# Performance work log

Measured on AMD Instinct MI355X. Metric: run time of the kernel, lower is better.

Reference implementation:

```python
import jax, jax.numpy as jnp
import numpy as np
import math

L, N, Q, C, H = 6, 32, 100, 256, 8


def setup_inputs() -> dict:
    key = jax.random.key(0)
    k0, k1, k2 = jax.random.split(key, 3)
    hs_pair = jax.random.normal(k0, (L, N, Q, C), jnp.float32)
    xb = math.sqrt(6.0 / (C + 3 * C))  # xavier_uniform bound for (3C, C)
    in_proj_w = jax.random.uniform(k1, (3 * C, C), jnp.float32, -xb, xb)
    in_proj_b = jnp.zeros((3 * C,), jnp.float32)
    ob = 1.0 / math.sqrt(C)  # nn.Linear default bound
    out_w = jax.random.uniform(k2, (C, C), jnp.float32, -ob, ob)
    out_b = jnp.zeros((C,), jnp.float32)
    return {"hs_pair": hs_pair, "in_proj_w": in_proj_w, "in_proj_b": in_proj_b,
            "out_w": out_w, "out_b": out_b}


def _smha(q, k, v, ipw, ipb, ow, ob, mask=None):
    """Sigmoid multi-head attention (SMHA), batch-first.
    q: (N,T,E), k/v: (N,S,E), mask: (T,S) bool (True = masked -> attn 0).
    Returns (out (N,T,E), head-averaged pre-normalization sigmoid weights (N,T,S))."""
    E = q.shape[-1]
    Dh = E // H
    Nb, T, _ = q.shape
    S = k.shape[1]
    wq, wk, wv = ipw[:E], ipw[E:2 * E], ipw[2 * E:]
    bq, bk, bv = ipb[:E], ipb[E:2 * E], ipb[2 * E:]
    qh = (q @ wq.T + bq).reshape(Nb, T, H, Dh)
    kh = (k @ wk.T + bk).reshape(Nb, S, H, Dh)
    vh = (v @ wv.T + bv).reshape(Nb, S, H, Dh)
    scores = jnp.einsum('nthd,nshd->nhts', qh, kh) / jnp.sqrt(jnp.asarray(Dh, qh.dtype))
    attn = jax.nn.sigmoid(scores)
    if mask is not None:
        attn = jnp.where(mask[None, None], 0.0, attn)  # sigmoid(-inf) == 0
    out = jnp.einsum('nhts,nshd->nthd', attn / (attn.sum(-1, keepdims=True) + 1e-4), vh)
    out = out.reshape(Nb, T, E) @ ow.T + ob
    return out, attn.mean(axis=1)


def _sqdist(a, b):
    # a (...,M,C), b (...,K,C) -> squared euclidean (...,M,K); avoids (M,K,C) diff tensor
    return jnp.maximum(jnp.sum(a * a, -1)[..., :, None] + jnp.sum(b * b, -1)[..., None, :]
                       - 2.0 * jnp.einsum('...mc,...kc->...mk', a, b), 0.0)


def _forward(hs_pair, ipw, ipb, ow, ob):
    hs = hs_pair[-1]  # (N,Q,C)
    Nb = hs.shape[0]

    # mean_farthest_assignment over all layers: centers (L,N,2,C)
    c1_all = hs_pair.mean(2, keepdims=True)                      # (L,N,1,C)
    d_all = _sqdist(c1_all, hs_pair)[..., 0, :]                  # (L,N,Q); sq dist preserves argmax
    far_all = jnp.argmax(d_all, -1)
    c2_all = jnp.take_along_axis(hs_pair, far_all[..., None, None], axis=2)
    centers = jnp.concatenate([c1_all, c2_all], 2)               # (L,N,2,C)

    # global field: 2 centers attend to Q pair features
    mf, assignment = _smha(centers[-1], hs, hs, ipw, ipb, ow, ob)  # (N,2,C), (N,2,Q)
    card = assignment.sum(-1)                                      # (N,2)
    s_idx = jnp.argmin(card, -1)
    d_idx = jnp.argmax(card, -1)
    cd = jnp.take_along_axis(mf, d_idx[:, None, None], 1)[:, 0]    # (N,C)
    cs = jnp.take_along_axis(mf, s_idx[:, None, None], 1)[:, 0]

    # base_idx row j = (j..j+Q-2) mod Q, i.e. it excludes (j-1) mod Q
    excl = (jnp.arange(Q) - 1) % Q
    sum_all = hs.sum(1)                                            # (N,C)
    rows = jnp.arange(Q)

    def branch(kv, c1):
        # kv (N,S,C); c1 (N,Q,C) leave-one-out means; returns shift (N,Q)
        S = kv.shape[1]
        d = _sqdist(c1, kv)                                        # (N,Q,S)
        em = jnp.arange(S)[None, :] == excl[:, None]               # exclude col (j-1)%Q
        far = jnp.argmax(jnp.where(em[None], -jnp.inf, d), -1)     # (N,Q)
        c2 = jnp.take_along_axis(kv, far[..., None], axis=1)       # (N,Q,C)
        cen = jnp.stack([c1, c2], 2).reshape(Nb, 2 * Q, C)         # interleaved [c1_j, c2_j]
        m = jnp.zeros((2 * Q, S), bool).at[2 * rows, rows].set(True).at[2 * rows + 1, rows].set(True)
        mfx, asg = _smha(cen, kv, kv, ipw, ipb, ow, ob, mask=m)    # (N,2Q,C), (N,2Q,S)
        mfx = mfx.reshape(Nb, Q, 2, C)
        asg = asg.reshape(Nb, Q, 2, S)
        cardx = asg.sum(-1)                                        # (N,Q,2)
        si = jnp.argmin(cardx, -1)
        di = jnp.argmax(cardx, -1)
        cdx = jnp.take_along_axis(mfx, di[..., None, None], 2)[:, :, 0]  # (N,Q,C)
        csx = jnp.take_along_axis(mfx, si[..., None, None], 2)[:, :, 0]
        return (jnp.sqrt(jnp.sum((cdx - cd[:, None]) ** 2, -1) + 1e-12)
                + jnp.sqrt(jnp.sum((csx - cs[:, None]) ** 2, -1) + 1e-12))

    # remove-one branch
    c1_rm = (sum_all[:, None] - hs[:, excl]) / (Q - 1)
    shift_rm = branch(hs, c1_rm)

    # mean-displace branch: subset + batch-mean pseudo point appended
    mean_pair = hs.mean(1, keepdims=True)                          # (N,1,C)
    kv_md = jnp.concatenate([hs, mean_pair], 1)                    # (N,Q+1,C)
    c1_md = (sum_all[:, None] - hs[:, excl] + mean_pair) / Q
    shift_md = branch(kv_md, c1_md)

    return assignment, s_idx, d_idx, shift_rm, shift_md


def reference(hs_pair, in_proj_w, in_proj_b, out_w, out_b):
    return _forward(hs_pair, in_proj_w, in_proj_b, out_w, out_b)
```

## Files before the change

kernel.cpp:

```cpp
#include <hip/hip_runtime.h>
#include <math.h>

#define NB 32
#define QQ 100
#define CC 256
#define HH 8
#define DH 32
#define SM 101
#define TT 200
#define TB 400
#define PW 768

typedef __attribute__((ext_vector_type(8))) short s16x8;
typedef __attribute__((ext_vector_type(4))) float f32x4;

__device__ inline unsigned short f2bft(float x) {
    return (unsigned short)(__float_as_uint(x) >> 16);
}
__device__ inline ushort2 tsplit(float x) {
    unsigned u = __float_as_uint(x);
    float l = x - __uint_as_float(u & 0xffff0000u);
    ushort2 r;
    r.x = (unsigned short)(u >> 16);
    r.y = (unsigned short)(__float_as_uint(l) >> 16);
    return r;
}

__global__ __launch_bounds__(256)
void meanrow_kernel(const float* __restrict__ hs, float* __restrict__ meanF) {
    int n = blockIdx.x, cb = blockIdx.y;
    int tid = threadIdx.x;
    int c = cb * 128 + (tid & 127), rh = tid >> 7;
    __shared__ float part[2][128];
    const float* h = hs + (size_t)n * QQ * CC;
    float s = 0.f;
    for (int q = rh * 50; q < rh * 50 + 50; ++q) s += h[(size_t)q * CC + c];
    part[rh][tid & 127] = s;
    __syncthreads();
    if (rh == 0) meanF[(size_t)n * CC + c] = (part[0][tid & 127] + part[1][tid & 127]) * 0.01f;
}

#define LDK 40
__global__ __launch_bounds__(256, 2)
void gemm_mfma(const float* __restrict__ hs, const float* __restrict__ meanF,
               const float* __restrict__ W_g, const float* __restrict__ bias,
               float* __restrict__ out, int M, int Nout) {
    __shared__ unsigned short Ahs[128][LDK], Als[128][LDK], Bhs[128][LDK], Bls[128][LDK];
    int tid = threadIdx.x;
    int lane = tid & 63, wave = tid >> 6;
    int wm = (wave >> 1) * 64, wn = (wave & 1) * 64;
    int fr = lane & 15, kb = lane >> 4;
    int bm = blockIdx.x * 128, bn = blockIdx.y * 128;
    int srow = tid >> 1, scol = (tid & 1) * 16;
    int am = bm + srow; if (am >= M) am = M - 1;
    int an = am / SM, ar = am - an * SM;
    const float* pA = (ar < QQ) ? hs + ((size_t)an * QQ + ar) * CC + scol
                                : meanF + (size_t)an * CC + scol;
    const float* pW = W_g + (size_t)(bn + srow) * CC + scol;
    f32x4 acc[4][4];
#pragma unroll
    for (int mi = 0; mi < 4; ++mi)
#pragma unroll
        for (int ni = 0; ni < 4; ++ni)
            acc[mi][ni] = (f32x4){0.f, 0.f, 0.f, 0.f};
    for (int k0 = 0; k0 < CC; k0 += 32) {
        float4 av[4], wv[4];
#pragma unroll
        for (int j = 0; j < 4; ++j) {
            av[j] = *(const float4*)(pA + k0 + 4 * j);
            wv[j] = *(const float4*)(pW + k0 + 4 * j);
        }
        __syncthreads();
#pragma unroll
        for (int j = 0; j < 4; ++j) {
            ushort2 sx = tsplit(av[j].x), sy = tsplit(av[j].y), sz = tsplit(av[j].z), sw = tsplit(av[j].w);
            ushort4 h4; h4.x = sx.x; h4.y = sy.x; h4.z = sz.x; h4.w = sw.x;
            ushort4 l4; l4.x = sx.y; l4.y = sy.y; l4.z = sz.y; l4.w = sw.y;
            *(ushort4*)&Ahs[srow][scol + 4 * j] = h4;
            *(ushort4*)&Als[srow][scol + 4 * j] = l4;
            ushort2 tx = tsplit(wv[j].x), ty = tsplit(wv[j].y), tz = tsplit(wv[j].z), tw = tsplit(wv[j].w);
            ushort4 wh4; wh4.x = tx.x; wh4.y = ty.x; wh4.z = tz.x; wh4.w = tw.x;
            ushort4 wl4; wl4.x = tx.y; wl4.y = ty.y; wl4.z = tz.y; wl4.w = tw.y;
            *(ushort4*)&Bhs[srow][scol + 4 * j] = wh4;
            *(ushort4*)&Bls[srow][scol + 4 * j] = wl4;
        }
        __syncthreads();
        s16x8 fah[4], fal[4], fbh[4], fbl[4];
#pragma unroll
        for (int mi = 0; mi < 4; ++mi) {
            fah[mi] = *(const s16x8*)&Ahs[wm + mi * 16 + fr][kb * 8];
            fal[mi] = *(const s16x8*)&Als[wm + mi * 16 + fr][kb * 8];
        }
#pragma unroll
        for (int ni = 0; ni < 4; ++ni) {
            fbh[ni] = *(const s16x8*)&Bhs[wn + ni * 16 + fr][kb * 8];
            fbl[ni] = *(const s16x8*)&Bls[wn + ni * 16 + fr][kb * 8];
        }
#pragma unroll
        for (int mi = 0; mi < 4; ++mi)
#pragma unroll
            for (int ni = 0; ni < 4; ++ni) {
                acc[mi][ni] = __builtin_amdgcn_mfma_f32_16x16x32_bf16(fah[mi], fbh[ni], acc[mi][ni], 0, 0, 0);
                acc[mi][ni] = __builtin_amdgcn_mfma_f32_16x16x32_bf16(fah[mi], fbl[ni], acc[mi][ni], 0, 0, 0);
                acc[mi][ni] = __builtin_amdgcn_mfma_f32_16x16x32_bf16(fal[mi], fbh[ni], acc[mi][ni], 0, 0, 0);
            }
    }
#pragma unroll
    for (int mi = 0; mi < 4; ++mi) {
        int mb = bm + wm + mi * 16 + kb * 4;
#pragma unroll
        for (int r = 0; r < 4; ++r) {
            int m = mb + r;
            if (m < M) {
#pragma unroll
                for (int ni = 0; ni < 4; ++ni) {
                    int col = bn + wn + ni * 16 + fr;
                    out[(size_t)m * Nout + col] = acc[mi][ni][r] + bias[col];
                }
            }
        }
    }
}

__global__ __launch_bounds__(512, 2)
void gramfar(const float* __restrict__ hs, const float* __restrict__ meanF,
             const float* __restrict__ P_all, float* __restrict__ Psum0,
             int* __restrict__ far0, int* __restrict__ far_rm,
             int* __restrict__ far_md) {
    int n = blockIdx.x;
    int tid = threadIdx.x;
    int wave = tid >> 6, lane = tid & 63;
    int fr = lane & 15, kb = lane >> 4;
    __shared__ float G[SM][104];
    __shared__ unsigned short Ah[112][LDK], Al[112][LDK];
    __shared__ float sumdot[104], meandot[104], norm[104];
    __shared__ float psumP[2][CC];
    {
        int c = tid & 255, half = tid >> 8;
        const float* basep = P_all + (size_t)n * SM * PW + c;
        float accp = 0.f;
        for (int q = half * 50; q < half * 50 + 50; ++q) accp += basep[(size_t)q * PW];
        psumP[half][c] = accp;
    }
    __syncthreads();
    if (tid < 256) Psum0[(size_t)n * CC + tid] = psumP[0][tid] + psumP[1][tid];
    const float* hb = hs + (size_t)n * QQ * CC;
    const float* mb = meanF + (size_t)n * CC;
    f32x4 acc[7];
#pragma unroll
    for (int u = 0; u < 7; ++u) acc[u] = (f32x4){0.f, 0.f, 0.f, 0.f};
    for (int k0 = 0; k0 < CC; k0 += 32) {
        __syncthreads();
        if (tid < 224) {
            int row = tid >> 1, kk = (tid & 1) * 16;
            float4 v[4];
            if (row < SM) {
                const float* rp = (row < QQ) ? hb + (size_t)row * CC : mb;
#pragma unroll
                for (int j = 0; j < 4; ++j) v[j] = *(const float4*)(rp + k0 + kk + 4 * j);
            } else {
#pragma unroll
                for (int j = 0; j < 4; ++j) v[j] = (float4){0.f, 0.f, 0.f, 0.f};
            }
#pragma unroll
            for (int j = 0; j < 4; ++j) {
                ushort2 sx = tsplit(v[j].x), sy = tsplit(v[j].y), sz = tsplit(v[j].z), sw = tsplit(v[j].w);
                ushort4 h4; h4.x = sx.x; h4.y = sy.x; h4.z = sz.x; h4.w = sw.x;
                ushort4 l4; l4.x = sx.y; l4.y = sy.y; l4.z = sz.y; l4.w = sw.y;
                *(ushort4*)&Ah[row][kk + 4 * j] = h4;
                *(ushort4*)&Al[row][kk + 4 * j] = l4;
            }
        }
        __syncthreads();
#pragma unroll
        for (int u = 0; u < 7; ++u) {
            int tl = wave + u * 8;
            if (tl < 49) {
                int ti = tl / 7, tj = tl % 7;
                s16x8 ah = *(const s16x8*)&Ah[ti * 16 + fr][kb * 8];
                s16x8 al = *(const s16x8*)&Al[ti * 16 + fr][kb * 8];
                s16x8 bh = *(const s16x8*)&Ah[tj * 16 + fr][kb * 8];
                s16x8 bl = *(const s16x8*)&Al[tj * 16 + fr][kb * 8];
                acc[u] = __builtin_amdgcn_mfma_f32_16x16x32_bf16(ah, bh, acc[u], 0, 0, 0);
                acc[u] = __builtin_amdgcn_mfma_f32_16x16x32_bf16(ah, bl, acc[u], 0, 0, 0);
                acc[u] = __builtin_amdgcn_mfma_f32_16x16x32_bf16(al, bh, acc[u], 0, 0, 0);
            }
        }
    }
    __syncthreads();
#pragma unroll
    for (int u = 0; u < 7; ++u) {
        int tl = wave + u * 8;
        if (tl < 49) {
            int ti = tl / 7, tj = tl % 7;
#pragma unroll
            for (int r = 0; r < 4; ++r) {
                int m = ti * 16 + kb * 4 + r;
                int col = tj * 16 + fr;
                if (m < SM && col < SM) G[m][col] = acc[u][r];
            }
        }
    }
    __syncthreads();
    for (int s = tid; s < SM; s += 512) {
        float a = 0.f;
        for (int q = 0; q < QQ; ++q) a += G[s][q];
        sumdot[s] = a; meandot[s] = G[s][QQ]; norm[s] = G[s][s];
    }
    __syncthreads();
    if (tid < QQ) {
        int q = tid, qm1 = (q + QQ - 1) % QQ;
        const float* gq = G[qm1];
        int best = -1; float bv = -1e30f;
        for (int s = 0; s < QQ; ++s) {
            if (s == qm1) continue;
            float val = norm[s] - (sumdot[s] - gq[s]) * (2.f / 99.f);
            if (val > bv) { bv = val; best = s; }
        }
        far_rm[n * QQ + q] = best;
    } else if (tid >= 128 && tid < 128 + QQ) {
        int q = tid - 128, qm1 = (q + QQ - 1) % QQ;
        const float* gq = G[qm1];
        int best = -1; float bv = -1e30f;
        for (int s = 0; s < SM; ++s) {
            if (s == qm1) continue;
            float val = norm[s] - (sumdot[s] - gq[s] + meandot[s]) * (2.f / 100.f);
            if (val > bv) { bv = val; best = s; }
        }
        far_md[n * QQ + q] = best;
    } else if (tid == 256) {
        int best = 0; float bv = -1e30f;
        for (int q = 0; q < QQ; ++q) {
            float val = norm[q] - 0.02f * sumdot[q];
            if (val > bv) { bv = val; best = q; }
        }
        far0[n] = best;
    }
}

__global__ __launch_bounds__(512)
void smhaB_kernel(const float* __restrict__ P_all, const int* __restrict__ far0,
                  const float* __restrict__ ow, const float* __restrict__ ob,
                  float* __restrict__ out_assign, float* __restrict__ out_sidx,
                  float* __restrict__ out_didx, float* __restrict__ cd,
                  float* __restrict__ cs) {
    int n = blockIdx.x;
    int tid = threadIdx.x;
    int h = tid >> 6, lane = tid & 63;
    __shared__ float at[HH][2][104];
    __shared__ float qsh[HH][2][DH];
    __shared__ float rsh[HH][2];
    __shared__ float pvs[2][CC];
    __shared__ int sdi[2];
    const float* base = P_all + (size_t)n * SM * PW;
    if (lane < 2 * DH) {
        int t = lane >> 5, d = lane & 31;
        int row = t ? far0[n] : QQ;
        qsh[h][t][d] = base[(size_t)row * PW + h * DH + d];
    }
    const float scl = 0.17677669529663687f;
    float p0 = 0.f, p1 = 0.f;
    for (int s = lane; s < 104; s += 64) {
        float a0v = 0.f, a1v = 0.f;
        if (s < QQ) {
            const float4* kr = (const float4*)(base + (size_t)s * PW + CC + h * DH);
            float d0 = 0.f, d1 = 0.f;
#pragma unroll
            for (int j = 0; j < 8; ++j) {
                float4 k4 = kr[j];
                d0 += qsh[h][0][4 * j] * k4.x + qsh[h][0][4 * j + 1] * k4.y
                    + qsh[h][0][4 * j + 2] * k4.z + qsh[h][0][4 * j + 3] * k4.w;
                d1 += qsh[h][1][4 * j] * k4.x + qsh[h][1][4 * j + 1] * k4.y
                    + qsh[h][1][4 * j + 2] * k4.z + qsh[h][1][4 * j + 3] * k4.w;
            }
            a0v = 1.f / (1.f + __expf(-d0 * scl));
            a1v = 1.f / (1.f + __expf(-d1 * scl));
            p0 += a0v; p1 += a1v;
        }
        at[h][0][s] = a0v;
        at[h][1][s] = a1v;
    }
#pragma unroll
    for (int off = 32; off > 0; off >>= 1) {
        p0 += __shfl_down(p0, off);
        p1 += __shfl_down(p1, off);
    }
    if (lane == 0) { rsh[h][0] = p0; rsh[h][1] = p1; }
    {
        int t = lane >> 5, d = lane & 31;
        float rv = (t ? p1 : p0);
        rv = __shfl(rv, 0);
        float inv = 1.f / (rv + 1e-4f);
        float acc = 0.f;
        const float* vb = base + 2 * CC + h * DH + d;
        for (int s = 0; s < QQ; ++s) acc += at[h][t][s] * vb[(size_t)s * PW];
        pvs[t][h * DH + d] = acc * inv;
    }
    __syncthreads();
    if (tid == 0) {
        float c0 = 0.f, c1v = 0.f;
        for (int h2 = 0; h2 < HH; ++h2) { c0 += rsh[h2][0]; c1v += rsh[h2][1]; }
        int si = (c1v < c0) ? 1 : 0;
        int di = (c1v > c0) ? 1 : 0;
        sdi[0] = si; sdi[1] = di;
        out_sidx[n] = (float)si;
        out_didx[n] = (float)di;
    }
    __syncthreads();
    if (tid < 2 * QQ) {
        int t = tid / QQ, s = tid % QQ;
        float m = 0.f;
#pragma unroll
        for (int h2 = 0; h2 < HH; ++h2) m += at[h2][t][s];
        out_assign[(size_t)n * 2 * QQ + tid] = m * 0.125f;
    }
    {
        int t = tid >> 8, c = tid & 255;
        const float4* wr4 = (const float4*)(ow + (size_t)c * CC);
        const float4* pz = (const float4*)&pvs[t][0];
        float a = ob[c];
#pragma unroll 8
        for (int k = 0; k < 64; ++k) {
            float4 w = wr4[k], x = pz[k];
            a += x.x * w.x + x.y * w.y + x.z * w.z + x.w * w.w;
        }
        if (t == sdi[1]) cd[(size_t)n * CC + c] = a;
        if (t == sdi[0]) cs[(size_t)n * CC + c] = a;
    }
}

__global__ __launch_bounds__(256)
void attn_mfma(const float* __restrict__ P_all, const float* __restrict__ Psum0,
               const int* __restrict__ far_rm, const int* __restrict__ far_md,
               float* __restrict__ pv, float* __restrict__ rowsum) {
    int h = blockIdx.x, n = blockIdx.y;
    int tid = threadIdx.x;
    int w = tid >> 6, lane = tid & 63;
    int fr = lane & 15, hi = lane >> 4;
    int d0 = hi * 8;
    __shared__ unsigned short Kh[112 * 40];
    __shared__ unsigned short Kl[112 * 40];
    __shared__ unsigned short Vt[32 * 136];
    __shared__ unsigned short Pb[4][64 * 40];
    __shared__ float rsL[4][112];
    const float* base = P_all + (size_t)n * SM * PW;
    for (int idx = tid; idx < 112 * 8; idx += 256) {
        int key = idx >> 3, d4 = (idx & 7) * 4;
        float4 kv = {0.f, 0.f, 0.f, 0.f}, vv = {0.f, 0.f, 0.f, 0.f};
        if (key < SM) {
            kv = *(const float4*)&base[(size_t)key * PW + CC + h * DH + d4];
            vv = *(const float4*)&base[(size_t)key * PW + 2 * CC + h * DH + d4];
        }
        ushort2 sx = tsplit(kv.x), sy = tsplit(kv.y), sz = tsplit(kv.z), sw = tsplit(kv.w);
        ushort4 h4; h4.x = sx.x; h4.y = sy.x; h4.z = sz.x; h4.w = sw.x;
        ushort4 l4; l4.x = sx.y; l4.y = sy.y; l4.z = sz.y; l4.w = sw.y;
        *(ushort4*)&Kh[key * 40 + d4] = h4;
        *(ushort4*)&Kl[key * 40 + d4] = l4;
        Vt[(d4 + 0) * 136 + key] = f2bft(vv.x);
        Vt[(d4 + 1) * 136 + key] = f2bft(vv.y);
        Vt[(d4 + 2) * 136 + key] = f2bft(vv.z);
        Vt[(d4 + 3) * 136 + key] = f2bft(vv.w);
    }
    for (int idx = tid; idx < 32 * 16; idx += 256) {
        int d = idx >> 4, key = 112 + (idx & 15);
        Vt[d * 136 + key] = 0;
    }
    __syncthreads();
    const float* Psum0n = Psum0 + n * CC;
    int rowbase = w * 100;
    unsigned short* Pw = Pb[w];
    const float scl = 0.17677669529663687f;
#pragma unroll
    for (int qg = 0; qg < 2; ++qg) {
        const int nq = qg ? 3 : 4;
        const int qt0 = qg * 4;
        s16x8 qh[4], ql[4];
        int mk[4], sb[4];
#pragma unroll
        for (int qi = 0; qi < 4; ++qi) {
            if (qi >= nq) { mk[qi] = -1; sb[qi] = 0; continue; }
            int lq = (qt0 + qi) * 16 + fr;
            int row = rowbase + (lq < QQ ? lq : QQ - 1);
            int b = row >= TT;
            int t = row - b * TT;
            int q = t >> 1;
            mk[qi] = q; sb[qi] = b ? SM : QQ;
            float qv[8];
            if (t & 1) {
                int f = (b ? far_md : far_rm)[n * QQ + q];
                const float4* pr = (const float4*)(base + (size_t)f * PW + h * DH + d0);
                float4 v0 = pr[0], v1 = pr[1];
                qv[0] = v0.x; qv[1] = v0.y; qv[2] = v0.z; qv[3] = v0.w;
                qv[4] = v1.x; qv[5] = v1.y; qv[6] = v1.z; qv[7] = v1.w;
            } else {
                int qm1 = (q + QQ - 1) % QQ;
                const float4* ps = (const float4*)(Psum0n + h * DH + d0);
                const float4* pm = (const float4*)(base + (size_t)qm1 * PW + h * DH + d0);
                const float4* pmn = (const float4*)(base + (size_t)QQ * PW + h * DH + d0);
                float invd = b ? 0.01f : (1.f / 99.f);
                float bb = b ? 1.f : 0.f;
                float4 a0 = ps[0], c0 = pm[0], m0 = pmn[0];
                float4 a1 = ps[1], c1 = pm[1], m1 = pmn[1];
                qv[0] = (a0.x - c0.x + bb * m0.x) * invd;
                qv[1] = (a0.y - c0.y + bb * m0.y) * invd;
                qv[2] = (a0.z - c0.z + bb * m0.z) * invd;
                qv[3] = (a0.w - c0.w + bb * m0.w) * invd;
                qv[4] = (a1.x - c1.x + bb * m1.x) * invd;
                qv[5] = (a1.y - c1.y + bb * m1.y) * invd;
                qv[6] = (a1.z - c1.z + bb * m1.z) * invd;
                qv[7] = (a1.w - c1.w + bb * m1.w) * invd;
            }
            s16x8 qhv, qlv;
#pragma unroll
            for (int j = 0; j < 8; ++j) {
                ushort2 sp = tsplit(qv[j]);
                qhv[j] = (short)sp.x;
                qlv[j] = (short)sp.y;
            }
            qh[qi] = qhv; ql[qi] = qlv;
        }
        f32x4 pvacc[4][2];
#pragma unroll
        for (int qi = 0; qi < 4; ++qi) {
            pvacc[qi][0] = (f32x4){0.f, 0.f, 0.f, 0.f};
            pvacc[qi][1] = (f32x4){0.f, 0.f, 0.f, 0.f};
        }
        float rs[4] = {0.f, 0.f, 0.f, 0.f};
#pragma unroll
        for (int kc = 0; kc < 4; ++kc) {
            int k0 = kc * 32;
            {
                s16x8 ah = *(const s16x8*)&Kh[(k0 + fr) * 40 + d0];
                s16x8 al = *(const s16x8*)&Kl[(k0 + fr) * 40 + d0];
#pragma unroll
                for (int qi = 0; qi < nq; ++qi) {
                    f32x4 s0 = (f32x4){0.f, 0.f, 0.f, 0.f};
                    s0 = __builtin_amdgcn_mfma_f32_16x16x32_bf16(ah, qh[qi], s0, 0, 0, 0);
                    s0 = __builtin_amdgcn_mfma_f32_16x16x32_bf16(ah, ql[qi], s0, 0, 0, 0);
                    s0 = __builtin_amdgcn_mfma_f32_16x16x32_bf16(al, qh[qi], s0, 0, 0, 0);
                    int kb0 = k0 + 4 * hi;
                    float a0 = (kb0 + 0 < sb[qi] && kb0 + 0 != mk[qi]) ? 1.f / (1.f + __expf(-s0[0] * scl)) : 0.f;
                    float a1 = (kb0 + 1 < sb[qi] && kb0 + 1 != mk[qi]) ? 1.f / (1.f + __expf(-s0[1] * scl)) : 0.f;
                    float a2 = (kb0 + 2 < sb[qi] && kb0 + 2 != mk[qi]) ? 1.f / (1.f + __expf(-s0[2] * scl)) : 0.f;
                    float a3 = (kb0 + 3 < sb[qi] && kb0 + 3 != mk[qi]) ? 1.f / (1.f + __expf(-s0[3] * scl)) : 0.f;
                    rs[qi] += a0 + a1 + a2 + a3;
                    ushort4 p4;
                    p4.x = f2bft(a0); p4.y = f2bft(a1); p4.z = f2bft(a2); p4.w = f2bft(a3);
                    *(ushort4*)&Pw[(qi * 16 + fr) * 40 + 4 * hi] = p4;
                }
            }
            if (kc < 3) {
                s16x8 ah = *(const s16x8*)&Kh[(k0 + 16 + fr) * 40 + d0];
                s16x8 al = *(const s16x8*)&Kl[(k0 + 16 + fr) * 40 + d0];
#pragma unroll
                for (int qi = 0; qi < nq; ++qi) {
                    f32x4 s1 = (f32x4){0.f, 0.f, 0.f, 0.f};
                    s1 = __builtin_amdgcn_mfma_f32_16x16x32_bf16(ah, qh[qi], s1, 0, 0, 0);
                    s1 = __builtin_amdgcn_mfma_f32_16x16x32_bf16(ah, ql[qi], s1, 0, 0, 0);
                    s1 = __builtin_amdgcn_mfma_f32_16x16x32_bf16(al, qh[qi], s1, 0, 0, 0);
                    int kb1 = k0 + 16 + 4 * hi;
                    float a0 = (kb1 + 0 < sb[qi] && kb1 + 0 != mk[qi]) ? 1.f / (1.f + __expf(-s1[0] * scl)) : 0.f;
                    float a1 = (kb1 + 1 < sb[qi] && kb1 + 1 != mk[qi]) ? 1.f / (1.f + __expf(-s1[1] * scl)) : 0.f;
                    float a2 = (kb1 + 2 < sb[qi] && kb1 + 2 != mk[qi]) ? 1.f / (1.f + __expf(-s1[2] * scl)) : 0.f;
                    float a3 = (kb1 + 3 < sb[qi] && kb1 + 3 != mk[qi]) ? 1.f / (1.f + __expf(-s1[3] * scl)) : 0.f;
                    rs[qi] += a0 + a1 + a2 + a3;
                    ushort4 p4;
                    p4.x = f2bft(a0); p4.y = f2bft(a1); p4.z = f2bft(a2); p4.w = f2bft(a3);
                    *(ushort4*)&Pw[(qi * 16 + fr) * 40 + 16 + 4 * hi] = p4;
                }
            } else {
                ushort4 z; z.x = 0; z.y = 0; z.z = 0; z.w = 0;
#pragma unroll
                for (int qi = 0; qi < nq; ++qi)
                    *(ushort4*)&Pw[(qi * 16 + fr) * 40 + 16 + 4 * hi] = z;
            }
            s16x8 vb0 = *(const s16x8*)&Vt[(0 * 16 + fr) * 136 + k0 + d0];
            s16x8 vb1 = *(const s16x8*)&Vt[(1 * 16 + fr) * 136 + k0 + d0];
#pragma unroll
            for (int qi = 0; qi < nq; ++qi) {
                s16x8 pa = *(const s16x8*)&Pw[(qi * 16 + fr) * 40 + d0];
                pvacc[qi][0] = __builtin_amdgcn_mfma_f32_16x16x32_bf16(pa, vb0, pvacc[qi][0], 0, 0, 0);
                pvacc[qi][1] = __builtin_amdgcn_mfma_f32_16x16x32_bf16(pa, vb1, pvacc[qi][1], 0, 0, 0);
            }
        }
#pragma unroll
        for (int qi = 0; qi < nq; ++qi) {
            float r2 = rs[qi] + __shfl_xor(rs[qi], 16);
            r2 += __shfl_xor(r2, 32);
            int lq = (qt0 + qi) * 16 + fr;
            if (hi == 0) {
                rsL[w][lq] = r2;
                if (lq < QQ) rowsum[((size_t)n * HH + h) * TB + rowbase + lq] = r2;
            }
        }
#pragma unroll
        for (int qi = 0; qi < nq; ++qi) {
            float iv[4];
#pragma unroll
            for (int r = 0; r < 4; ++r) {
                int lq = (qt0 + qi) * 16 + 4 * hi + r;
                iv[r] = 1.f / (rsL[w][lq < 112 ? lq : 111] + 1e-4f);
            }
#pragma unroll
            for (int dt = 0; dt < 2; ++dt) {
#pragma unroll
                for (int r = 0; r < 4; ++r) {
                    int lq = (qt0 + qi) * 16 + 4 * hi + r;
                    if (lq < QQ)
                        pv[((size_t)n * TB + rowbase + lq) * CC + h * DH + dt * 16 + fr] = pvacc[qi][dt][r] * iv[r];
                }
            }
        }
    }
}

__global__ __launch_bounds__(512)
void outshift(const float* __restrict__ pv, const float* __restrict__ ow,
              const float* __restrict__ ob, const float* __restrict__ cd,
              const float* __restrict__ cs, const float* __restrict__ rowsum,
              float* __restrict__ out_srm, float* __restrict__ out_smd) {
    __shared__ unsigned short Ahs[64][LDK], Als[64][LDK];
    __shared__ unsigned short Bhs[256][LDK], Bls[256][LDK];
    __shared__ float redcd[64][8], redcs[64][8];
    int tid = threadIdx.x;
    int lane = tid & 63, wave = tid >> 6;
    int wn = wave * 32;
    int fr = lane & 15, kb = lane >> 4;
    int bm = blockIdx.x * 64;
    int arow = tid >> 3, ak = (tid & 7) * 4;
    int brow = tid >> 1, bk = (tid & 1) * 16;
    const float* pA = pv + (size_t)(bm + arow) * CC + ak;
    const float* pB = ow + (size_t)brow * CC + bk;
    f32x4 acc[4][2];
#pragma unroll
    for (int mi = 0; mi < 4; ++mi)
#pragma unroll
        for (int ni = 0; ni < 2; ++ni)
            acc[mi][ni] = (f32x4){0.f, 0.f, 0.f, 0.f};
    for (int k0 = 0; k0 < CC; k0 += 32) {
        float4 av = *(const float4*)(pA + k0);
        float4 wv[4];
#pragma unroll
        for (int j = 0; j < 4; ++j) wv[j] = *(const float4*)(pB + k0 + 4 * j);
        __syncthreads();
        {
            ushort2 sx = tsplit(av.x), sy = tsplit(av.y), sz = tsplit(av.z), sw = tsplit(av.w);
            ushort4 h4; h4.x = sx.x; h4.y = sy.x; h4.z = sz.x; h4.w = sw.x;
            ushort4 l4; l4.x = sx.y; l4.y = sy.y; l4.z = sz.y; l4.w = sw.y;
            *(ushort4*)&Ahs[arow][ak] = h4;
            *(ushort4*)&Als[arow][ak] = l4;
        }
#pragma unroll
        for (int j = 0; j < 4; ++j) {
            ushort2 sx = tsplit(wv[j].x), sy = tsplit(wv[j].y), sz = tsplit(wv[j].z), sw = tsplit(wv[j].w);
            ushort4 h4; h4.x = sx.x; h4.y = sy.x; h4.z = sz.x; h4.w = sw.x;
            ushort4 l4; l4.x = sx.y; l4.y = sy.y; l4.z = sz.y; l4.w = sw.y;
            *(ushort4*)&Bhs[brow][bk + 4 * j] = h4;
            *(ushort4*)&Bls[brow][bk + 4 * j] = l4;
        }
        __syncthreads();
        s16x8 fah[4], fal[4], fbh[2], fbl[2];
#pragma unroll
        for (int mi = 0; mi < 4; ++mi) {
            fah[mi] = *(const s16x8*)&Ahs[mi * 16 + fr][kb * 8];
            fal[mi] = *(const s16x8*)&Als[mi * 16 + fr][kb * 8];
        }
#pragma unroll
        for (int ni = 0; ni < 2; ++ni) {
            fbh[ni] = *(const s16x8*)&Bhs[wn + ni * 16 + fr][kb * 8];
            fbl[ni] = *(const s16x8*)&Bls[wn + ni * 16 + fr][kb * 8];
        }
#pragma unroll
        for (int mi = 0; mi < 4; ++mi)
#pragma unroll
            for (int ni = 0; ni < 2; ++ni) {
                acc[mi][ni] = __builtin_amdgcn_mfma_f32_16x16x32_bf16(fah[mi], fbh[ni], acc[mi][ni], 0, 0, 0);
                acc[mi][ni] = __builtin_amdgcn_mfma_f32_16x16x32_bf16(fah[mi], fbl[ni], acc[mi][ni], 0, 0, 0);
                acc[mi][ni] = __builtin_amdgcn_mfma_f32_16x16x32_bf16(fal[mi], fbh[ni], acc[mi][ni], 0, 0, 0);
            }
    }
#pragma unroll
    for (int mi = 0; mi < 4; ++mi) {
#pragma unroll
        for (int r = 0; r < 4; ++r) {
            int lm = mi * 16 + kb * 4 + r;
            int g = bm + lm;
            int n = g / TB;
            float pcd = 0.f, pcs = 0.f;
#pragma unroll
            for (int ni = 0; ni < 2; ++ni) {
                int col = wn + ni * 16 + fr;
                float val = acc[mi][ni][r] + ob[col];
                float d1 = val - cd[(size_t)n * CC + col];
                float d2 = val - cs[(size_t)n * CC + col];
                pcd += d1 * d1;
                pcs += d2 * d2;
            }
#pragma unroll
            for (int m2 = 1; m2 < 16; m2 <<= 1) {
                pcd += __shfl_xor(pcd, m2);
                pcs += __shfl_xor(pcs, m2);
            }
            if (fr == 0) {
                redcd[lm][wave] = pcd;
                redcs[lm][wave] = pcs;
            }
        }
    }
    __syncthreads();
    if (tid < 32) {
        int g = bm + 2 * tid;
        int n = g / TB;
        int rem = g % TB;
        int b = rem / TT;
        int t = rem % TT;
        int q = t >> 1;
        float c0 = 0.f, c1v = 0.f;
        for (int h = 0; h < HH; ++h) {
            c0  += rowsum[((size_t)n * HH + h) * TB + rem];
            c1v += rowsum[((size_t)n * HH + h) * TB + rem + 1];
        }
        int si = (c1v < c0) ? 1 : 0;
        int di = (c1v > c0) ? 1 : 0;
        int ld = 2 * tid + di, ls = 2 * tid + si;
        float dd = 0.f, ds = 0.f;
#pragma unroll
        for (int wv2 = 0; wv2 < 8; ++wv2) { dd += redcd[ld][wv2]; ds += redcs[ls][wv2]; }
        (b ? out_smd : out_srm)[n * QQ + q] = sqrtf(dd + 1e-12f) + sqrtf(ds + 1e-12f);
    }
}

extern "C" void kernel_launch(void* const* d_in, const int* in_sizes, int n_in,
                              void* d_out, int out_size, void* d_ws, size_t ws_size,
                              hipStream_t stream) {
    const float* hs_pair = (const float*)d_in[0];
    const float* ipw = (const float*)d_in[1];
    const float* ipb = (const float*)d_in[2];
    const float* ow  = (const float*)d_in[3];
    const float* ob  = (const float*)d_in[4];
    const float* hs = hs_pair + (size_t)5 * NB * QQ * CC;

    float* ws = (float*)d_ws;
    size_t o = 0;
    float* meanF   = ws + o; o += NB * CC;
    float* P_all   = ws + o; o += (size_t)NB * SM * PW;
    float* Psum0   = ws + o; o += NB * CC;
    int*   far0    = (int*)(ws + o); o += NB;
    int*   far_rm  = (int*)(ws + o); o += NB * QQ;
    int*   far_md  = (int*)(ws + o); o += NB * QQ;
    float* cd      = ws + o; o += NB * CC;
    float* cs      = ws + o; o += NB * CC;
    float* pv      = ws + o; o += (size_t)NB * TB * CC;
    float* rowsum  = ws + o; o += (size_t)NB * HH * TB;
    if (o * sizeof(float) > ws_size) return;

    float* out = (float*)d_out;
    float* out_assign = out;
    float* out_sidx   = out + 6400;
    float* out_didx   = out + 6432;
    float* out_srm    = out + 6464;
    float* out_smd    = out + 9664;

    meanrow_kernel<<<dim3(NB, 2), 256, 0, stream>>>(hs, meanF);
    gemm_mfma<<<dim3((NB * SM + 127) / 128, PW / 128), 256, 0, stream>>>(
        hs, meanF, ipw, ipb, P_all, NB * SM, PW);
    gramfar<<<NB, 512, 0, stream>>>(hs, meanF, P_all, Psum0, far0, far_rm, far_md);
    smhaB_kernel<<<NB, 512, 0, stream>>>(P_all, far0, ow, ob, out_assign,
                                         out_sidx, out_didx, cd, cs);
    attn_mfma<<<dim3(HH, NB), 256, 0, stream>>>(P_all, Psum0, far_rm, far_md, pv, rowsum);
    outshift<<<NB * TB / 64, 512, 0, stream>>>(pv, ow, ob, cd, cs, rowsum, out_srm, out_smd);
}
```

Measured before the change: 119.7 us.

## Split Gram kernel into row-strip blocks and widen attention to eight waves

The single-block-per-batch Gram plus farthest-selection kernel is split in two. A 7xN grid computes the Gram matrix in 16-row strips and writes it to global memory, and a separate small kernel does the row sums and the argmax selections. The attention kernel now runs 8 waves per block, each handling 50 rows instead of 100, to spread the per-head work across more waves. The attention-probability and V conversion to bf16 now rounds to nearest instead of truncating. In exchange this adds an extra launch and a global round trip for G.

```diff
diff --git a/kernel.cpp b/kernel.cpp
--- a/kernel.cpp
+++ b/kernel.cpp
@@ -14,9 +14,6 @@
 typedef __attribute__((ext_vector_type(8))) short s16x8;
 typedef __attribute__((ext_vector_type(4))) float f32x4;
 
-__device__ inline unsigned short f2bft(float x) {
-    return (unsigned short)(__float_as_uint(x) >> 16);
-}
 __device__ inline ushort2 tsplit(float x) {
     unsigned u = __float_as_uint(x);
     float l = x - __uint_as_float(u & 0xffff0000u);
@@ -24,6 +21,10 @@
     r.x = (unsigned short)(u >> 16);
     r.y = (unsigned short)(__float_as_uint(l) >> 16);
     return r;
+}
+__device__ inline unsigned short f2bf(float x) {
+    unsigned u = __float_as_uint(x);
+    return (unsigned short)((u + 0x7fffu + ((u >> 16) & 1u)) >> 16);
 }
 
 __global__ __launch_bounds__(256)
@@ -122,33 +123,20 @@
     }
 }
 
-__global__ __launch_bounds__(512, 2)
-void gramfar(const float* __restrict__ hs, const float* __restrict__ meanF,
-             const float* __restrict__ P_all, float* __restrict__ Psum0,
-             int* __restrict__ far0, int* __restrict__ far_rm,
-             int* __restrict__ far_md) {
-    int n = blockIdx.x;
+__global__ __launch_bounds__(256, 2)
+void gram_strip(const float* __restrict__ hs, const float* __restrict__ meanF,
+                float* __restrict__ G) {
+    int ti = blockIdx.x, n = blockIdx.y;
     int tid = threadIdx.x;
     int wave = tid >> 6, lane = tid & 63;
     int fr = lane & 15, kb = lane >> 4;
-    __shared__ float G[SM][104];
     __shared__ unsigned short Ah[112][LDK], Al[112][LDK];
-    __shared__ float sumdot[104], meandot[104], norm[104];
-    __shared__ float psumP[2][CC];
-    {
-        int c = tid & 255, half = tid >> 8;
-        const float* basep = P_all + (size_t)n * SM * PW + c;
-        float accp = 0.f;
-        for (int q = half * 50; q < half * 50 + 50; ++q) accp += basep[(size_t)q * PW];
-        psumP[half][c] = accp;
-    }
-    __syncthreads();
-    if (tid < 256) Psum0[(size_t)n * CC + tid] = psumP[0][tid] + psumP[1][tid];
     const float* hb = hs + (size_t)n * QQ * CC;
     const float* mb = meanF + (size_t)n * CC;
-    f32x4 acc[7];
-#pragma unroll
-    for (int u = 0; u < 7; ++u) acc[u] = (f32x4){0.f, 0.f, 0.f, 0.f};
+    f32x4 acc[2];
+    acc[0] = (f32x4){0.f, 0.f, 0.f, 0.f};
+    acc[1] = (f32x4){0.f, 0.f, 0.f, 0.f};
+    int tj0 = wave, tj1 = wave + 4;
     for (int k0 = 0; k0 < CC; k0 += 32) {
         __syncthreads();
         if (tid < 224) {
@@ -172,45 +160,61 @@
             }
         }
         __syncthreads();
-#pragma unroll
-        for (int u = 0; u < 7; ++u) {
-            int tl = wave + u * 8;
-            if (tl < 49) {
-                int ti = tl / 7, tj = tl % 7;
-                s16x8 ah = *(const s16x8*)&Ah[ti * 16 + fr][kb * 8];
-                s16x8 al = *(const s16x8*)&Al[ti * 16 + fr][kb * 8];
-                s16x8 bh = *(const s16x8*)&Ah[tj * 16 + fr][kb * 8];
-                s16x8 bl = *(const s16x8*)&Al[tj * 16 + fr][kb * 8];
-                acc[u] = __builtin_amdgcn_mfma_f32_16x16x32_bf16(ah, bh, acc[u], 0, 0, 0);
-                acc[u] = __builtin_amdgcn_mfma_f32_16x16x32_bf16(ah, bl, acc[u], 0, 0, 0);
-                acc[u] = __builtin_amdgcn_mfma_f32_16x16x32_bf16(al, bh, acc[u], 0, 0, 0);
-            }
-        }
-    }
-    __syncthreads();
-#pragma unroll
-    for (int u = 0; u < 7; ++u) {
-        int tl = wave + u * 8;
-        if (tl < 49) {
-            int ti = tl / 7, tj = tl % 7;
-#pragma unroll
-            for (int r = 0; r < 4; ++r) {
-                int m = ti * 16 + kb * 4 + r;
-                int col = tj * 16 + fr;
-                if (m < SM && col < SM) G[m][col] = acc[u][r];
-            }
-        }
-    }
-    __syncthreads();
-    for (int s = tid; s < SM; s += 512) {
+        s16x8 ah = *(const s16x8*)&Ah[ti * 16 + fr][kb * 8];
+        s16x8 al = *(const s16x8*)&Al[ti * 16 + fr][kb * 8];
+        {
+            s16x8 bh = *(const s16x8*)&Ah[tj0 * 16 + fr][kb * 8];
+            s16x8 bl = *(const s16x8*)&Al[tj0 * 16 + fr][kb * 8];
+            acc[0] = __builtin_amdgcn_mfma_f32_16x16x32_bf16(ah, bh, acc[0], 0, 0, 0);
+            acc[0] = __builtin_amdgcn_mfma_f32_16x16x32_bf16(ah, bl, acc[0], 0, 0, 0);
+            acc[0] = __builtin_amdgcn_mfma_f32_16x16x32_bf16(al, bh, acc[0], 0, 0, 0);
+        }
+        if (tj1 < 7) {
+            s16x8 bh = *(const s16x8*)&Ah[tj1 * 16 + fr][kb * 8];
+            s16x8 bl = *(const s16x8*)&Al[tj1 * 16 + fr][kb * 8];
+            acc[1] = __builtin_amdgcn_mfma_f32_16x16x32_bf16(ah, bh, acc[1], 0, 0, 0);
+            acc[1] = __builtin_amdgcn_mfma_f32_16x16x32_bf16(ah, bl, acc[1], 0, 0, 0);
+            acc[1] = __builtin_amdgcn_mfma_f32_16x16x32_bf16(al, bh, acc[1], 0, 0, 0);
+        }
+    }
+    float* Gn = G + (size_t)n * SM * 104;
+#pragma unroll
+    for (int u = 0; u < 2; ++u) {
+        int tj = u ? tj1 : tj0;
+        if (tj >= 7) continue;
+#pragma unroll
+        for (int r = 0; r < 4; ++r) {
+            int m = ti * 16 + kb * 4 + r;
+            int col = tj * 16 + fr;
+            if (m < SM && col < SM) Gn[(size_t)m * 104 + col] = (u ? acc[1] : acc[0])[r];
+        }
+    }
+}
+
+__global__ __launch_bounds__(256)
+void farsel(const float* __restrict__ G, const float* __restrict__ P_all,
+            float* __restrict__ Psum0, int* __restrict__ far0,
+            int* __restrict__ far_rm, int* __restrict__ far_md) {
+    int n = blockIdx.x;
+    int tid = threadIdx.x;
+    __shared__ float sumdot[104], meandot[104], norm[104];
+    const float* Gn = G + (size_t)n * SM * 104;
+    {
+        const float* basep = P_all + (size_t)n * SM * PW + tid;
+        float accp = 0.f;
+        for (int q = 0; q < QQ; ++q) accp += basep[(size_t)q * PW];
+        Psum0[(size_t)n * CC + tid] = accp;
+    }
+    if (tid < SM) {
+        const float* row = Gn + (size_t)tid * 104;
         float a = 0.f;
-        for (int q = 0; q < QQ; ++q) a += G[s][q];
-        sumdot[s] = a; meandot[s] = G[s][QQ]; norm[s] = G[s][s];
+        for (int q = 0; q < QQ; ++q) a += row[q];
+        sumdot[tid] = a; meandot[tid] = row[QQ]; norm[tid] = row[tid];
     }
     __syncthreads();
     if (tid < QQ) {
         int q = tid, qm1 = (q + QQ - 1) % QQ;
-        const float* gq = G[qm1];
+        const float* gq = Gn + (size_t)qm1 * 104;
         int best = -1; float bv = -1e30f;
         for (int s = 0; s < QQ; ++s) {
             if (s == qm1) continue;
@@ -220,7 +224,7 @@
         far_rm[n * QQ + q] = best;
     } else if (tid >= 128 && tid < 128 + QQ) {
         int q = tid - 128, qm1 = (q + QQ - 1) % QQ;
-        const float* gq = G[qm1];
+        const float* gq = Gn + (size_t)qm1 * 104;
         int best = -1; float bv = -1e30f;
         for (int s = 0; s < SM; ++s) {
             if (s == qm1) continue;
@@ -228,7 +232,7 @@
             if (val > bv) { bv = val; best = s; }
         }
         far_md[n * QQ + q] = best;
-    } else if (tid == 256) {
+    } else if (tid == 100) {
         int best = 0; float bv = -1e30f;
         for (int q = 0; q < QQ; ++q) {
             float val = norm[q] - 0.02f * sumdot[q];
@@ -329,7 +333,7 @@
     }
 }
 
-__global__ __launch_bounds__(256)
+__global__ __launch_bounds__(512)
 void attn_mfma(const float* __restrict__ P_all, const float* __restrict__ Psum0,
                const int* __restrict__ far_rm, const int* __restrict__ far_md,
                float* __restrict__ pv, float* __restrict__ rowsum) {
@@ -341,10 +345,10 @@
     __shared__ unsigned short Kh[112 * 40];
     __shared__ unsigned short Kl[112 * 40];
     __shared__ unsigned short Vt[32 * 136];
-    __shared__ unsigned short Pb[4][64 * 40];
-    __shared__ float rsL[4][112];
+    __shared__ unsigned short Pb[8][64 * 40];
+    __shared__ float rsL[8][64];
     const float* base = P_all + (size_t)n * SM * PW;
-    for (int idx = tid; idx < 112 * 8; idx += 256) {
+    for (int idx = tid; idx < 112 * 8; idx += 512) {
         int key = idx >> 3, d4 = (idx & 7) * 4;
         float4 kv = {0.f, 0.f, 0.f, 0.f}, vv = {0.f, 0.f, 0.f, 0.f};
         if (key < SM) {
@@ -356,159 +360,153 @@
         ushort4 l4; l4.x = sx.y; l4.y = sy.y; l4.z = sz.y; l4.w = sw.y;
         *(ushort4*)&Kh[key * 40 + d4] = h4;
         *(ushort4*)&Kl[key * 40 + d4] = l4;
-        Vt[(d4 + 0) * 136 + key] = f2bft(vv.x);
-        Vt[(d4 + 1) * 136 + key] = f2bft(vv.y);
-        Vt[(d4 + 2) * 136 + key] = f2bft(vv.z);
-        Vt[(d4 + 3) * 136 + key] = f2bft(vv.w);
-    }
-    for (int idx = tid; idx < 32 * 16; idx += 256) {
+        Vt[(d4 + 0) * 136 + key] = f2bf(vv.x);
+        Vt[(d4 + 1) * 136 + key] = f2bf(vv.y);
+        Vt[(d4 + 2) * 136 + key] = f2bf(vv.z);
+        Vt[(d4 + 3) * 136 + key] = f2bf(vv.w);
+    }
+    for (int idx = tid; idx < 32 * 16; idx += 512) {
         int d = idx >> 4, key = 112 + (idx & 15);
         Vt[d * 136 + key] = 0;
     }
     __syncthreads();
     const float* Psum0n = Psum0 + n * CC;
-    int rowbase = w * 100;
+    int rowbase = w * 50;
     unsigned short* Pw = Pb[w];
     const float scl = 0.17677669529663687f;
-#pragma unroll
-    for (int qg = 0; qg < 2; ++qg) {
-        const int nq = qg ? 3 : 4;
-        const int qt0 = qg * 4;
-        s16x8 qh[4], ql[4];
-        int mk[4], sb[4];
+    s16x8 qh[4], ql[4];
+    int mk[4], sb[4];
+#pragma unroll
+    for (int qi = 0; qi < 4; ++qi) {
+        int lq = qi * 16 + fr;
+        int row = rowbase + (lq < 50 ? lq : 49);
+        int b = row >= TT;
+        int t = row - b * TT;
+        int q = t >> 1;
+        mk[qi] = q; sb[qi] = b ? SM : QQ;
+        float qv[8];
+        if (t & 1) {
+            int f = (b ? far_md : far_rm)[n * QQ + q];
+            const float4* pr = (const float4*)(base + (size_t)f * PW + h * DH + d0);
+            float4 v0 = pr[0], v1 = pr[1];
+            qv[0] = v0.x; qv[1] = v0.y; qv[2] = v0.z; qv[3] = v0.w;
+            qv[4] = v1.x; qv[5] = v1.y; qv[6] = v1.z; qv[7] = v1.w;
+        } else {
+            int qm1 = (q + QQ - 1) % QQ;
+            const float4* ps = (const float4*)(Psum0n + h * DH + d0);
+            const float4* pm = (const float4*)(base + (size_t)qm1 * PW + h * DH + d0);
+            const float4* pmn = (const float4*)(base + (size_t)QQ * PW + h * DH + d0);
+            float invd = b ? 0.01f : (1.f / 99.f);
+            float bb = b ? 1.f : 0.f;
+            float4 a0 = ps[0], c0 = pm[0], m0 = pmn[0];
+            float4 a1 = ps[1], c1 = pm[1], m1 = pmn[1];
+            qv[0] = (a0.x - c0.x + bb * m0.x) * invd;
+            qv[1] = (a0.y - c0.y + bb * m0.y) * invd;
+            qv[2] = (a0.z - c0.z + bb * m0.z) * invd;
+            qv[3] = (a0.w - c0.w + bb * m0.w) * invd;
+            qv[4] = (a1.x - c1.x + bb * m1.x) * invd;
+            qv[5] = (a1.y - c1.y + bb * m1.y) * invd;
+            qv[6] = (a1.z - c1.z + bb * m1.z) * invd;
+            qv[7] = (a1.w - c1.w + bb * m1.w) * invd;
+        }
+        s16x8 qhv, qlv;
+#pragma unroll
+        for (int j = 0; j < 8; ++j) {
+            ushort2 sp = tsplit(qv[j]);
+            qhv[j] = (short)sp.x;
+            qlv[j] = (short)sp.y;
+        }
+        qh[qi] = qhv; ql[qi] = qlv;
+    }
+    f32x4 pvacc[4][2];
+#pragma unroll
+    for (int qi = 0; qi < 4; ++qi) {
+        pvacc[qi][0] = (f32x4){0.f, 0.f, 0.f, 0.f};
+        pvacc[qi][1] = (f32x4){0.f, 0.f, 0.f, 0.f};
+    }
+    float rs[4] = {0.f, 0.f, 0.f, 0.f};
+#pragma unroll
+    for (int kc = 0; kc < 4; ++kc) {
+        int k0 = kc * 32;
+        {
+            s16x8 ah = *(const s16x8*)&Kh[(k0 + fr) * 40 + d0];
+            s16x8 al = *(const s16x8*)&Kl[(k0 + fr) * 40 + d0];
+#pragma unroll
+            for (int qi = 0; qi < 4; ++qi) {
+                f32x4 s0 = (f32x4){0.f, 0.f, 0.f, 0.f};
+                s0 = __builtin_amdgcn_mfma_f32_16x16x32_bf16(ah, qh[qi], s0, 0, 0, 0);
+                s0 = __builtin_amdgcn_mfma_f32_16x16x32_bf16(ah, ql[qi], s0, 0, 0, 0);
+                s0 = __builtin_amdgcn_mfma_f32_16x16x32_bf16(al, qh[qi], s0, 0, 0, 0);
+                int kb0 = k0 + 4 * hi;
+                float a0 = (kb0 + 0 < sb[qi] && kb0 + 0 != mk[qi]) ? 1.f / (1.f + __expf(-s0[0] * scl)) : 0.f;
+                float a1 = (kb0 + 1 < sb[qi] && kb0 + 1 != mk[qi]) ? 1.f / (1.f + __expf(-s0[1] * scl)) : 0.f;
+                float a2 = (kb0 + 2 < sb[qi] && kb0 + 2 != mk[qi]) ? 1.f / (1.f + __expf(-s0[2] * scl)) : 0.f;
+                float a3 = (kb0 + 3 < sb[qi] && kb0 + 3 != mk[qi]) ? 1.f / (1.f + __expf(-s0[3] * scl)) : 0.f;
+                rs[qi] += a0 + a1 + a2 + a3;
+                ushort4 p4;
+                p4.x = f2bf(a0); p4.y = f2bf(a1); p4.z = f2bf(a2); p4.w = f2bf(a3);
+                *(ushort4*)&Pw[(qi * 16 + fr) * 40 + 4 * hi] = p4;
+            }
+        }
+        if (kc < 3) {
+            s16x8 ah = *(const s16x8*)&Kh[(k0 + 16 + fr) * 40 + d0];
+            s16x8 al = *(const s16x8*)&Kl[(k0 + 16 + fr) * 40 + d0];
+#pragma unroll
+            for (int qi = 0; qi < 4; ++qi) {
+                f32x4 s1 = (f32x4){0.f, 0.f, 0.f, 0.f};
+                s1 = __builtin_amdgcn_mfma_f32_16x16x32_bf16(ah, qh[qi], s1, 0, 0, 0);
+                s1 = __builtin_amdgcn_mfma_f32_16x16x32_bf16(ah, ql[qi], s1, 0, 0, 0);
+                s1 = __builtin_amdgcn_mfma_f32_16x16x32_bf16(al, qh[qi], s1, 0, 0, 0);
+                int kb1 = k0 + 16 + 4 * hi;
+                float a0 = (kb1 + 0 < sb[qi] && kb1 + 0 != mk[qi]) ? 1.f / (1.f + __expf(-s1[0] * scl)) : 0.f;
+                float a1 = (kb1 + 1 < sb[qi] && kb1 + 1 != mk[qi]) ? 1.f / (1.f + __expf(-s1[1] * scl)) : 0.f;
+                float a2 = (kb1 + 2 < sb[qi] && kb1 + 2 != mk[qi]) ? 1.f / (1.f + __expf(-s1[2] * scl)) : 0.f;
+                float a3 = (kb1 + 3 < sb[qi] && kb1 + 3 != mk[qi]) ? 1.f / (1.f + __expf(-s1[3] * scl)) : 0.f;
+                rs[qi] += a0 + a1 + a2 + a3;
+                ushort4 p4;
+                p4.x = f2bf(a0); p4.y = f2bf(a1); p4.z = f2bf(a2); p4.w = f2bf(a3);
+                *(ushort4*)&Pw[(qi * 16 + fr) * 40 + 16 + 4 * hi] = p4;
+            }
+        } else {
+            ushort4 z; z.x = 0; z.y = 0; z.z = 0; z.w = 0;
+#pragma unroll
+            for (int qi = 0; qi < 4; ++qi)
+                *(ushort4*)&Pw[(qi * 16 + fr) * 40 + 16 + 4 * hi] = z;
+        }
+        s16x8 vb0 = *(const s16x8*)&Vt[(0 * 16 + fr) * 136 + k0 + d0];
+        s16x8 vb1 = *(const s16x8*)&Vt[(1 * 16 + fr) * 136 + k0 + d0];
 #pragma unroll
         for (int qi = 0; qi < 4; ++qi) {
-            if (qi >= nq) { mk[qi] = -1; sb[qi] = 0; continue; }
-            int lq = (qt0 + qi) * 16 + fr;
-            int row = rowbase + (lq < QQ ? lq : QQ - 1);
-            int b = row >= TT;
-            int t = row - b * TT;
-            int q = t >> 1;
-            mk[qi] = q; sb[qi] = b ? SM : QQ;
-            float qv[8];
-            if (t & 1) {
-                int f = (b ? far_md : far_rm)[n * QQ + q];
-                const float4* pr = (const float4*)(base + (size_t)f * PW + h * DH + d0);
-                float4 v0 = pr[0], v1 = pr[1];
-                qv[0] = v0.x; qv[1] = v0.y; qv[2] = v0.z; qv[3] = v0.w;
-                qv[4] = v1.x; qv[5] = v1.y; qv[6] = v1.z; qv[7] = v1.w;
-            } else {
-                int qm1 = (q + QQ - 1) % QQ;
-                const float4* ps = (const float4*)(Psum0n + h * DH + d0);
-                const float4* pm = (const float4*)(base + (size_t)qm1 * PW + h * DH + d0);
-                const float4* pmn = (const float4*)(base + (size_t)QQ * PW + h * DH + d0);
-                float invd = b ? 0.01f : (1.f / 99.f);
-                float bb = b ? 1.f : 0.f;
-                float4 a0 = ps[0], c0 = pm[0], m0 = pmn[0];
-                float4 a1 = ps[1], c1 = pm[1], m1 = pmn[1];
-                qv[0] = (a0.x - c0.x + bb * m0.x) * invd;
-                qv[1] = (a0.y - c0.y + bb * m0.y) * invd;
-                qv[2] = (a0.z - c0.z + bb * m0.z) * invd;
-                qv[3] = (a0.w - c0.w + bb * m0.w) * invd;
-                qv[4] = (a1.x - c1.x + bb * m1.x) * invd;
-                qv[5] = (a1.y - c1.y + bb * m1.y) * invd;
-                qv[6] = (a1.z - c1.z + bb * m1.z) * invd;
-                qv[7] = (a1.w - c1.w + bb * m1.w) * invd;
-            }
-            s16x8 qhv, qlv;
-#pragma unroll
-            for (int j = 0; j < 8; ++j) {
-                ushort2 sp = tsplit(qv[j]);
-                qhv[j] = (short)sp.x;
-                qlv[j] = (short)sp.y;
-            }
-            qh[qi] = qhv; ql[qi] = qlv;
-        }
-        f32x4 pvacc[4][2];
-#pragma unroll
-        for (int qi = 0; qi < 4; ++qi) {
-            pvacc[qi][0] = (f32x4){0.f, 0.f, 0.f, 0.f};
-            pvacc[qi][1] = (f32x4){0.f, 0.f, 0.f, 0.f};
-        }
-        float rs[4] = {0.f, 0.f, 0.f, 0.f};
-#pragma unroll
-        for (int kc = 0; kc < 4; ++kc) {
-            int k0 = kc * 32;
-            {
-                s16x8 ah = *(const s16x8*)&Kh[(k0 + fr) * 40 + d0];
-                s16x8 al = *(const s16x8*)&Kl[(k0 + fr) * 40 + d0];
-#pragma unroll
-                for (int qi = 0; qi < nq; ++qi) {
-                    f32x4 s0 = (f32x4){0.f, 0.f, 0.f, 0.f};
-                    s0 = __builtin_amdgcn_mfma_f32_16x16x32_bf16(ah, qh[qi], s0, 0, 0, 0);
-                    s0 = __builtin_amdgcn_mfma_f32_16x16x32_bf16(ah, ql[qi], s0, 0, 0, 0);
-                    s0 = __builtin_amdgcn_mfma_f32_16x16x32_bf16(al, qh[qi], s0, 0, 0, 0);
-                    int kb0 = k0 + 4 * hi;
-                    float a0 = (kb0 + 0 < sb[qi] && kb0 + 0 != mk[qi]) ? 1.f / (1.f + __expf(-s0[0] * scl)) : 0.f;
-                    float a1 = (kb0 + 1 < sb[qi] && kb0 + 1 != mk[qi]) ? 1.f / (1.f + __expf(-s0[1] * scl)) : 0.f;
-                    float a2 = (kb0 + 2 < sb[qi] && kb0 + 2 != mk[qi]) ? 1.f / (1.f + __expf(-s0[2] * scl)) : 0.f;
-                    float a3 = (kb0 + 3 < sb[qi] && kb0 + 3 != mk[qi]) ? 1.f / (1.f + __expf(-s0[3] * scl)) : 0.f;
-                    rs[qi] += a0 + a1 + a2 + a3;
-                    ushort4 p4;
-                    p4.x = f2bft(a0); p4.y = f2bft(a1); p4.z = f2bft(a2); p4.w = f2bft(a3);
-                    *(ushort4*)&Pw[(qi * 16 + fr) * 40 + 4 * hi] = p4;
-                }
-            }
-            if (kc < 3) {
-                s16x8 ah = *(const s16x8*)&Kh[(k0 + 16 + fr) * 40 + d0];
-                s16x8 al = *(const s16x8*)&Kl[(k0 + 16 + fr) * 40 + d0];
-#pragma unroll
-                for (int qi = 0; qi < nq; ++qi) {
-                    f32x4 s1 = (f32x4){0.f, 0.f, 0.f, 0.f};
-                    s1 = __builtin_amdgcn_mfma_f32_16x16x32_bf16(ah, qh[qi], s1, 0, 0, 0);
-                    s1 = __builtin_amdgcn_mfma_f32_16x16x32_bf16(ah, ql[qi], s1, 0, 0, 0);
-                    s1 = __builtin_amdgcn_mfma_f32_16x16x32_bf16(al, qh[qi], s1, 0, 0, 0);
-                    int kb1 = k0 + 16 + 4 * hi;
-                    float a0 = (kb1 + 0 < sb[qi] && kb1 + 0 != mk[qi]) ? 1.f / (1.f + __expf(-s1[0] * scl)) : 0.f;
-                    float a1 = (kb1 + 1 < sb[qi] && kb1 + 1 != mk[qi]) ? 1.f / (1.f + __expf(-s1[1] * scl)) : 0.f;
-                    float a2 = (kb1 + 2 < sb[qi] && kb1 + 2 != mk[qi]) ? 1.f / (1.f + __expf(-s1[2] * scl)) : 0.f;
-                    float a3 = (kb1 + 3 < sb[qi] && kb1 + 3 != mk[qi]) ? 1.f / (1.f + __expf(-s1[3] * scl)) : 0.f;
-                    rs[qi] += a0 + a1 + a2 + a3;
-                    ushort4 p4;
-                    p4.x = f2bft(a0); p4.y = f2bft(a1); p4.z = f2bft(a2); p4.w = f2bft(a3);
-                    *(ushort4*)&Pw[(qi * 16 + fr) * 40 + 16 + 4 * hi] = p4;
-                }
-            } else {
-                ushort4 z; z.x = 0; z.y = 0; z.z = 0; z.w = 0;
-#pragma unroll
-                for (int qi = 0; qi < nq; ++qi)
-                    *(ushort4*)&Pw[(qi * 16 + fr) * 40 + 16 + 4 * hi] = z;
-            }
-            s16x8 vb0 = *(const s16x8*)&Vt[(0 * 16 + fr) * 136 + k0 + d0];
-            s16x8 vb1 = *(const s16x8*)&Vt[(1 * 16 + fr) * 136 + k0 + d0];
-#pragma unroll
-            for (int qi = 0; qi < nq; ++qi) {
-                s16x8 pa = *(const s16x8*)&Pw[(qi * 16 + fr) * 40 + d0];
-                pvacc[qi][0] = __builtin_amdgcn_mfma_f32_16x16x32_bf16(pa, vb0, pvacc[qi][0], 0, 0, 0);
-                pvacc[qi][1] = __builtin_amdgcn_mfma_f32_16x16x32_bf16(pa, vb1, pvacc[qi][1], 0, 0, 0);
-            }
-        }
-#pragma unroll
-        for (int qi = 0; qi < nq; ++qi) {
-            float r2 = rs[qi] + __shfl_xor(rs[qi], 16);
-            r2 += __shfl_xor(r2, 32);
-            int lq = (qt0 + qi) * 16 + fr;
-            if (hi == 0) {
-                rsL[w][lq] = r2;
-                if (lq < QQ) rowsum[((size_t)n * HH + h) * TB + rowbase + lq] = r2;
-            }
-        }
-#pragma unroll
-        for (int qi = 0; qi < nq; ++qi) {
-            float iv[4];
+            s16x8 pa = *(const s16x8*)&Pw[(qi * 16 + fr) * 40 + d0];
+            pvacc[qi][0] = __builtin_amdgcn_mfma_f32_16x16x32_bf16(pa, vb0, pvacc[qi][0], 0, 0, 0);
+            pvacc[qi][1] = __builtin_amdgcn_mfma_f32_16x16x32_bf16(pa, vb1, pvacc[qi][1], 0, 0, 0);
+        }
+    }
+#pragma unroll
+    for (int qi = 0; qi < 4; ++qi) {
+        float r2 = rs[qi] + __shfl_xor(rs[qi], 16);
+        r2 += __shfl_xor(r2, 32);
+        int lq = qi * 16 + fr;
+        if (hi == 0) {
+            rsL[w][lq] = r2;
+            if (lq < 50) rowsum[((size_t)n * HH + h) * TB + rowbase + lq] = r2;
+        }
+    }
+#pragma unroll
+    for (int qi = 0; qi < 4; ++qi) {
+        float iv[4];
+#pragma unroll
+        for (int r = 0; r < 4; ++r) {
+            int lq = qi * 16 + 4 * hi + r;
+            iv[r] = 1.f / (rsL[w][lq] + 1e-4f);
+        }
+#pragma unroll
+        for (int dt = 0; dt < 2; ++dt) {
 #pragma unroll
             for (int r = 0; r < 4; ++r) {
-                int lq = (qt0 + qi) * 16 + 4 * hi + r;
-                iv[r] = 1.f / (rsL[w][lq < 112 ? lq : 111] + 1e-4f);
-            }
-#pragma unroll
-            for (int dt = 0; dt < 2; ++dt) {
-#pragma unroll
-                for (int r = 0; r < 4; ++r) {
-                    int lq = (qt0 + qi) * 16 + 4 * hi + r;
-                    if (lq < QQ)
-                        pv[((size_t)n * TB + rowbase + lq) * CC + h * DH + dt * 16 + fr] = pvacc[qi][dt][r] * iv[r];
-                }
+                int lq = qi * 16 + 4 * hi + r;
+                if (lq < 50)
+                    pv[((size_t)n * TB + rowbase + lq) * CC + h * DH + dt * 16 + fr] = pvacc[qi][dt][r] * iv[r];
             }
         }
     }
@@ -645,6 +643,7 @@
     float* meanF   = ws + o; o += NB * CC;
     float* P_all   = ws + o; o += (size_t)NB * SM * PW;
     float* Psum0   = ws + o; o += NB * CC;
+    float* G       = ws + o; o += (size_t)NB * SM * 104;
     int*   far0    = (int*)(ws + o); o += NB;
     int*   far_rm  = (int*)(ws + o); o += NB * QQ;
     int*   far_md  = (int*)(ws + o); o += NB * QQ;
@@ -664,9 +663,10 @@
     meanrow_kernel<<<dim3(NB, 2), 256, 0, stream>>>(hs, meanF);
     gemm_mfma<<<dim3((NB * SM + 127) / 128, PW / 128), 256, 0, stream>>>(
         hs, meanF, ipw, ipb, P_all, NB * SM, PW);
-    gramfar<<<NB, 512, 0, stream>>>(hs, meanF, P_all, Psum0, far0, far_rm, far_md);
+    gram_strip<<<dim3(7, NB), 256, 0, stream>>>(hs, meanF, G);
+    farsel<<<NB, 256, 0, stream>>>(G, P_all, Psum0, far0, far_rm, far_md);
     smhaB_kernel<<<NB, 512, 0, stream>>>(P_all, far0, ow, ob, out_assign,
                                          out_sidx, out_didx, cd, cs);
-    attn_mfma<<<dim3(HH, NB), 256, 0, stream>>>(P_all, Psum0, far_rm, far_md, pv, rowsum);
+    attn_mfma<<<dim3(HH, NB), 512, 0, stream>>>(P_all, Psum0, far_rm, far_md, pv, rowsum);
     outshift<<<NB * TB / 64, 512, 0, stream>>>(pv, ow, ob, cd, cs, rowsum, out_srm, out_smd);
 }
```

After: 116.8 us. 1.02x faster.
